# Kernel tuning notes

Measured on AMD Instinct MI355X. Metric: run time of the kernel, lower is better.

Reference implementation:

```python
import jax, jax.numpy as jnp
import numpy as np

B, L, D = 2, 2048, 1024
H, G = 16, 2            # num_heads, num_kv_groups
HPG = H // G            # heads per kv group = 8
DQK, DV = 128, 128      # qk_head_dim, v_head_dim (head_dim=64, ratios=2.0)


def setup_inputs() -> dict:
    key = jax.random.key(0)
    ks = jax.random.split(key, 12)

    def xavier(k, shape, scale=1.0):
        fan_in, fan_out = shape[0], shape[1]
        lim = np.sqrt(6.0 / (fan_in + fan_out))
        return jax.random.uniform(k, shape, jnp.float32, -lim, lim) * scale

    return {
        "in_q": jax.random.normal(ks[0], (B, L, D), jnp.float32),
        "in_k": jax.random.normal(ks[1], (B, L, D), jnp.float32),
        "in_v": jax.random.normal(ks[2], (B, L, D), jnp.float32),
        # weights stored as [in, out] (transpose of torch Linear); qk_init_scale=0.5
        "Wq": xavier(ks[3], (D, H * DQK), 0.5),
        "bq": jnp.zeros((H * DQK,), jnp.float32),
        "Wk": xavier(ks[4], (D, G * DQK), 0.5),
        "bk": jnp.zeros((G * DQK,), jnp.float32),
        "Wv": xavier(ks[5], (D, G * DV)),
        "bv": jnp.zeros((G * DV,), jnp.float32),
        "Wo": xavier(ks[6], (H * DV, D)),
        "bo": jnp.zeros((D,), jnp.float32),
        "q_extra_scale": jnp.ones((1,), jnp.float32),
    }


def reference(in_q, in_k, in_v, Wq, bq, Wk, bk, Wv, bv, Wo, bo, q_extra_scale):
    # fused projections
    q = (in_q @ Wq + bq) * q_extra_scale              # [B,L,H*DQK]
    k = in_k @ Wk + bk                                 # [B,L,G*DQK]
    v = in_v @ Wv + bv                                 # [B,L,G*DV]

    # reshape: keep GQA group structure instead of materializing repeat_interleave
    q = q.reshape(B, L, G, HPG, DQK)                   # heads grouped: head h = g*HPG + m
    k = k.reshape(B, L, G, DQK)
    v = v.reshape(B, L, G, DV)

    scale = 1.0 / np.sqrt(DQK)
    # scores: [B,G,HPG,L_q,L_kv]
    scores = jnp.einsum("bsgmd,btgd->bgmst", q, k) * scale
    causal = jnp.tril(jnp.ones((L, L), bool))          # is_causal=True
    scores = jnp.where(causal, scores, jnp.finfo(scores.dtype).min)
    attn = jax.nn.softmax(scores, axis=-1)
    ctx = jnp.einsum("bgmst,btgd->bsgmd", attn, v)     # [B,L,G,HPG,DV]
    ctx = ctx.reshape(B, L, H * DV)
    return ctx @ Wo + bo                               # [B,L,D]
```

## Files before the change

### kernel.cpp

```cpp
#include <hip/hip_runtime.h>


typedef __bf16 bf16;
typedef __bf16 bf16x8 __attribute__((ext_vector_type(8)));
typedef __bf16 bf16x4 __attribute__((ext_vector_type(4)));
typedef float f32x4 __attribute__((ext_vector_type(4)));
typedef float float4v __attribute__((ext_vector_type(4)));

#define MFMA_BF16(a, b, c) __builtin_amdgcn_mfma_f32_16x16x32_bf16((a), (b), (c), 0, 0, 0)

static constexpr int Bz = 2, Lz = 2048, Dz = 1024;
static constexpr int Hz = 16, Gz = 2;
static constexpr int DQKz = 128, DVz = 128;

__device__ __forceinline__ void async_copy16(const bf16* g, bf16* l) {
    __builtin_amdgcn_global_load_lds(
        (const __attribute__((address_space(1))) unsigned int*)g,
        (__attribute__((address_space(3))) unsigned int*)l, 16, 0, 0);
}

__global__ __launch_bounds__(256) void prep(
    const float* __restrict__ q, const float* __restrict__ k,
    const float* __restrict__ v, bf16* __restrict__ dq,
    bf16* __restrict__ dk, bf16* __restrict__ dv,
    const float* __restrict__ Wq, const float* __restrict__ Wk,
    const float* __restrict__ Wv, const float* __restrict__ Wo,
    bf16* __restrict__ WqT, bf16* __restrict__ WkT,
    bf16* __restrict__ WvT, bf16* __restrict__ WoT)
{
    int bid = blockIdx.x;
    if (bid < 6144) {
        const float* s = bid < 2048 ? q : (bid < 4096 ? k : v);
        bf16* d = bid < 2048 ? dq : (bid < 4096 ? dk : dv);
        int i = (bid & 2047) * 2048 + threadIdx.x * 8;
        float4v a = *(const float4v*)(s + i);
        float4v b = *(const float4v*)(s + i + 4);
        bf16x8 o;
        #pragma unroll
        for (int j = 0; j < 4; ++j) { o[j] = (bf16)a[j]; o[j + 4] = (bf16)b[j]; }
        *(bf16x8*)(d + i) = o;
        return;
    }
    bid -= 6144;
    const float* W; bf16* WT; int K, N;
    if (bid < 2048)      { W = Wq; WT = WqT; K = 1024; N = 2048; }
    else if (bid < 2304) { W = Wk; WT = WkT; K = 1024; N = 256;  bid -= 2048; }
    else if (bid < 2560) { W = Wv; WT = WvT; K = 1024; N = 256;  bid -= 2304; }
    else                 { W = Wo; WT = WoT; K = 2048; N = 1024; bid -= 2560; }
    int tiles_n = N >> 5;
    int n0 = (bid % tiles_n) * 32, k0 = (bid / tiles_n) * 32;

    __shared__ bf16 t[32][33];
    int tx = threadIdx.x & 31, ty = threadIdx.x >> 5;
    #pragma unroll
    for (int i = 0; i < 4; ++i)
        t[ty + i * 8][tx] = (bf16)W[(size_t)(k0 + ty + i * 8) * N + n0 + tx];
    __syncthreads();
    #pragma unroll
    for (int i = 0; i < 4; ++i)
        WT[(size_t)(n0 + ty + i * 8) * K + k0 + tx] = t[tx][ty + i * 8];
}

template <typename TC>
__device__ __forceinline__ void gemm_tile(
    const bf16* __restrict__ A, const bf16* __restrict__ BT,
    const float* __restrict__ bias, float scale, TC* __restrict__ C,
    int M, int N, int K, int m0, int n0, bool trans_out,
    bf16 (&As)[2][128 * 64], bf16 (&Bs)[2][128 * 64])
{
    const int tid  = threadIdx.x;
    const int wave = tid >> 6;
    const int lane = tid & 63;
    const int quad = lane >> 4;
    const int l16  = lane & 15;
    const int sw   = l16 & 7;
    const int wm = wave >> 2, wn = wave & 3;

    f32x4 acc[4][2] = {};

    auto stage = [&](int k0, int buf) {
        #pragma unroll
        for (int s = 0; s < 2; ++s) {
            int i = s * 512 + tid;
            int row = i >> 3, c = (i & 7) ^ (row & 7);
            async_copy16(A + (size_t)(m0 + row) * K + k0 + c * 8, &As[buf][i * 8]);
        }
        #pragma unroll
        for (int s = 0; s < 2; ++s) {
            int i = s * 512 + tid;
            int row = i >> 3, c = (i & 7) ^ (row & 7);
            async_copy16(BT + (size_t)(n0 + row) * K + k0 + c * 8, &Bs[buf][i * 8]);
        }
    };

    stage(0, 0);
    int cur = 0;
    for (int k0 = 0; k0 < K; k0 += 64) {
        __syncthreads();
        if (k0 + 64 < K) stage(k0 + 64, cur ^ 1);

        #pragma unroll
        for (int ks = 0; ks < 2; ++ks) {
            bf16x8 af[4], bfv[2];
            #pragma unroll
            for (int mt = 0; mt < 4; ++mt)
                af[mt] = *(const bf16x8*)(&As[cur][((wm * 64 + mt * 16 + l16) * 8
                                                    + ((ks * 4 + quad) ^ sw)) * 8]);
            #pragma unroll
            for (int nt = 0; nt < 2; ++nt)
                bfv[nt] = *(const bf16x8*)(&Bs[cur][((wn * 32 + nt * 16 + l16) * 8
                                                     + ((ks * 4 + quad) ^ sw)) * 8]);
            #pragma unroll
            for (int mt = 0; mt < 4; ++mt)
                #pragma unroll
                for (int nt = 0; nt < 2; ++nt)
                    acc[mt][nt] = MFMA_BF16(af[mt], bfv[nt], acc[mt][nt]);
        }
        cur ^= 1;
    }

    #pragma unroll
    for (int nt = 0; nt < 2; ++nt) {
        int col = n0 + wn * 32 + nt * 16 + l16;
        float bv = bias[col];
        #pragma unroll
        for (int mt = 0; mt < 4; ++mt) {
            int row = m0 + wm * 64 + mt * 16 + quad * 4;
            if (trans_out) {
                struct V4 { TC v[4]; } o;
                #pragma unroll
                for (int r = 0; r < 4; ++r)
                    o.v[r] = (TC)((acc[mt][nt][r] + bv) * scale);
                *(V4*)(&C[(size_t)col * M + row]) = o;
            } else {
                #pragma unroll
                for (int r = 0; r < 4; ++r)
                    C[(size_t)(row + r) * N + col] =
                        (TC)((acc[mt][nt][r] + bv) * scale);
            }
        }
    }
}

__global__ __launch_bounds__(512, 4) void proj_qkv(
    const bf16* __restrict__ aq, const bf16* __restrict__ ak,
    const bf16* __restrict__ av, const bf16* __restrict__ WqT,
    const bf16* __restrict__ WkT, const bf16* __restrict__ WvT,
    const float* __restrict__ bq, const float* __restrict__ bk,
    const float* __restrict__ bv, const float* __restrict__ qsc,
    bf16* __restrict__ Qw, bf16* __restrict__ Kw, bf16* __restrict__ VwT)
{
    __shared__ bf16 As[2][128 * 64];
    __shared__ bf16 Bs[2][128 * 64];
    int bid = blockIdx.x;
    if (bid < 512) {
        float scale = qsc[0] * 0.08838834764831845f * 1.4426950408889634f;
        gemm_tile<bf16>(aq, WqT, bq, scale, Qw, 4096, 2048, 1024,
                        (bid >> 4) * 128, (bid & 15) * 128, false, As, Bs);
    } else if (bid < 576) {
        int b2 = bid - 512;
        gemm_tile<bf16>(ak, WkT, bk, 1.0f, Kw, 4096, 256, 1024,
                        (b2 >> 1) * 128, (b2 & 1) * 128, false, As, Bs);
    } else {
        int b2 = bid - 576;
        gemm_tile<bf16>(av, WvT, bv, 1.0f, VwT, 4096, 256, 1024,
                        (b2 >> 1) * 128, (b2 & 1) * 128, true, As, Bs);
    }
}

__global__ __launch_bounds__(512, 4) void proj_o(
    const bf16* __restrict__ Cw, const bf16* __restrict__ WoT,
    const float* __restrict__ bo, float* __restrict__ out)
{
    __shared__ bf16 As[2][128 * 64];
    __shared__ bf16 Bs[2][128 * 64];
    gemm_tile<float>(Cw, WoT, bo, 1.0f, out, 4096, 1024, 2048,
                     (blockIdx.x >> 3) * 128, (blockIdx.x & 7) * 128,
                     false, As, Bs);
}

__global__ __launch_bounds__(256, 2) void attn_fused(
    const bf16* __restrict__ Q,
    const bf16* __restrict__ Kp,
    const bf16* __restrict__ VT,
    bf16* __restrict__ ctx)
{
    __shared__ bf16 Kb[2][64 * 128];
    __shared__ bf16 Vb[2][128 * 64];
    __shared__ bf16 Ps[4][16 * 72];

    const int tid  = threadIdx.x;
    const int wave = tid >> 6;
    const int lane = tid & 63;
    const int quad = lane >> 4;
    const int l16  = lane & 15;
    const int sw   = l16 & 7;

    const int h = blockIdx.y;
    const int b = blockIdx.z;
    const int g = h >> 3;

    const bf16* kgbase = Kp + (size_t)(b * Lz) * (Gz * DQKz) + g * DQKz;
    const bf16* vgbase = VT + (size_t)(g * DVz) * (Bz * Lz) + b * Lz;

    auto stage = [&](int kt, int buf) {
        const bf16* kb = kgbase + (size_t)(kt * 64) * (Gz * DQKz);
        #pragma unroll
        for (int s = 0; s < 4; ++s) {
            int i = s * 256 + tid;
            int key = i >> 4, c = (i & 15) ^ (key & 7);
            async_copy16(kb + (size_t)key * (Gz * DQKz) + c * 8, &Kb[buf][i * 8]);
        }
        const bf16* vb = vgbase + kt * 64;
        #pragma unroll
        for (int s = 0; s < 4; ++s) {
            int i = s * 256 + tid;
            int dv = i >> 3, c = (i & 7) ^ (dv & 7);
            async_copy16(vb + (size_t)dv * (Bz * Lz) + c * 8, &Vb[buf][i * 8]);
        }
    };

    for (int pass = 0; pass < 2; ++pass) {
        const int qt  = pass == 0 ? (31 - blockIdx.x) : blockIdx.x;
        const int q0  = qt * 64;
        const int nkt = qt + 1;
        const int qrow = q0 + wave * 16 + l16;

        bf16x8 qf[4];
        {
            const bf16* qbase = Q + (size_t)(b * Lz + qrow) * (Hz * DQKz) + h * DQKz;
            #pragma unroll
            for (int ks = 0; ks < 4; ++ks)
                qf[ks] = *(const bf16x8*)(qbase + ks * 32 + quad * 8);
        }

        f32x4 oacc[8] = {};
        float lsum = 0.0f;

        if (pass) __syncthreads();
        stage(0, 0);
        int cur = 0;

        bf16* ps = Ps[wave];

        for (int kt = 0; kt < nkt; ++kt) {
            __syncthreads();
            if (kt + 1 < nkt) stage(kt + 1, cur ^ 1);

            const bf16* kcur = Kb[cur];
            const bf16* vcur = Vb[cur];

            f32x4 sacc[4] = {};
            #pragma unroll
            for (int nf = 0; nf < 4; ++nf) {
                #pragma unroll
                for (int ks = 0; ks < 4; ++ks) {
                    bf16x8 kf = *(const bf16x8*)(&kcur[((nf * 16 + l16) * 16
                                                        + ((ks * 4 + quad) ^ sw)) * 8]);
                    sacc[nf] = MFMA_BF16(kf, qf[ks], sacc[nf]);
                }
            }

            float pv[4][4];
            if (kt == nkt - 1) {
                const int kv0 = kt * 64;
                #pragma unroll
                for (int nf = 0; nf < 4; ++nf) {
                    int keyb = kv0 + nf * 16 + quad * 4;
                    #pragma unroll
                    for (int r = 0; r < 4; ++r)
                        pv[nf][r] = (keyb + r > qrow) ? 0.0f
                                                      : exp2f(sacc[nf][r] - 8.0f);
                }
            } else {
                #pragma unroll
                for (int nf = 0; nf < 4; ++nf)
                    #pragma unroll
                    for (int r = 0; r < 4; ++r)
                        pv[nf][r] = exp2f(sacc[nf][r] - 8.0f);
            }

            #pragma unroll
            for (int nf = 0; nf < 4; ++nf)
                lsum += (pv[nf][0] + pv[nf][1]) + (pv[nf][2] + pv[nf][3]);

            #pragma unroll
            for (int nf = 0; nf < 4; ++nf) {
                bf16x4 pk;
                #pragma unroll
                for (int r = 0; r < 4; ++r) pk[r] = (bf16)pv[nf][r];
                *(bf16x4*)(&ps[l16 * 72 + nf * 16 + quad * 4]) = pk;
            }

            #pragma unroll
            for (int ks2 = 0; ks2 < 2; ++ks2) {
                bf16x8 pf = *(const bf16x8*)(&ps[l16 * 72 + ks2 * 32 + quad * 8]);
                #pragma unroll
                for (int nf2 = 0; nf2 < 8; ++nf2) {
                    bf16x8 vf = *(const bf16x8*)(&vcur[((nf2 * 16 + l16) * 8
                                                        + ((ks2 * 4 + quad) ^ sw)) * 8]);
                    oacc[nf2] = MFMA_BF16(vf, pf, oacc[nf2]);
                }
            }
            cur ^= 1;
        }

        lsum += __shfl_xor(lsum, 16);
        lsum += __shfl_xor(lsum, 32);
        const float inv = 1.0f / lsum;

        bf16* cbase = ctx + (size_t)(b * Lz + qrow) * (Hz * DVz) + h * DVz;
        #pragma unroll
        for (int nf2 = 0; nf2 < 8; ++nf2) {
            bf16x4 o4;
            #pragma unroll
            for (int r = 0; r < 4; ++r) o4[r] = (bf16)(oacc[nf2][r] * inv);
            *(bf16x4*)(&cbase[nf2 * 16 + quad * 4]) = o4;
        }
    }
}

extern "C" void kernel_launch(void* const* d_in, const int* in_sizes, int n_in,
                              void* d_out, int out_size, void* d_ws, size_t ws_size,
                              hipStream_t stream)
{
    (void)in_sizes; (void)n_in; (void)out_size; (void)ws_size;

    const float* in_q = (const float*)d_in[0];
    const float* in_k = (const float*)d_in[1];
    const float* in_v = (const float*)d_in[2];
    const float* Wq   = (const float*)d_in[3];
    const float* bq   = (const float*)d_in[4];
    const float* Wk   = (const float*)d_in[5];
    const float* bk   = (const float*)d_in[6];
    const float* Wv   = (const float*)d_in[7];
    const float* bv   = (const float*)d_in[8];
    const float* Wo   = (const float*)d_in[9];
    const float* bo   = (const float*)d_in[10];
    const float* qsc  = (const float*)d_in[11];
    float* out = (float*)d_out;

    const int M = Bz * Lz;
    const int NQ = Hz * DQKz;
    const int NKV = Gz * DQKz;

    bf16* aq  = (bf16*)d_ws;
    bf16* WqT = aq  + (size_t)M * Dz;
    bf16* WkT = WqT + (size_t)NQ * Dz;
    bf16* WvT = WkT + (size_t)NKV * Dz;
    bf16* WoT = WvT + (size_t)NKV * Dz;
    bf16* Qw  = WoT + (size_t)Dz * NQ;
    bf16* Kw  = Qw  + (size_t)M * NQ;
    bf16* VwT = Kw  + (size_t)M * NKV;
    bf16* Cw  = VwT + (size_t)NKV * M;
    bf16* ak  = Cw;
    bf16* av  = Cw + (size_t)M * Dz;

    prep<<<dim3(10752), dim3(256), 0, stream>>>(
        in_q, in_k, in_v, aq, ak, av, Wq, Wk, Wv, Wo, WqT, WkT, WvT, WoT);

    proj_qkv<<<dim3(640), dim3(512), 0, stream>>>(
        aq, ak, av, WqT, WkT, WvT, bq, bk, bv, qsc, Qw, Kw, VwT);

    attn_fused<<<dim3(Lz / 128, Hz, Bz), dim3(256), 0, stream>>>(Qw, Kw, VwT, Cw);

    proj_o<<<dim3(256), dim3(512), 0, stream>>>(Cw, WoT, bo, out);
}
```

Baseline: 256.4 us.

## Share K/V tiles across four heads per attention block, add XCD-aware GEMM tile mapping

The attention kernel now runs 512 threads per block. Each block covers four heads of one KV group over 32 query rows, so every K/V tile staged into LDS is reused by four heads instead of one. This cuts global and LDS staging traffic per head. The P scratch buffer switches from padding to an XOR swizzle to avoid bank conflicts, and the Q and O projection GEMMs remap block IDs so neighbouring M tiles land on the same XCD for L2 reuse. In exchange, the tighter launch bounds (512,4) could force register spills, and the grid has fewer, larger blocks.

```diff
diff --git a/kernel.cpp b/kernel.cpp
--- a/kernel.cpp
+++ b/kernel.cpp
@@ -154,9 +154,12 @@
     __shared__ bf16 Bs[2][128 * 64];
     int bid = blockIdx.x;
     if (bid < 512) {
+        int xcd = bid & 7, rest = bid >> 3;
+        int n = rest & 15, mg = rest >> 4;
+        int m = mg * 8 + xcd;
         float scale = qsc[0] * 0.08838834764831845f * 1.4426950408889634f;
         gemm_tile<bf16>(aq, WqT, bq, scale, Qw, 4096, 2048, 1024,
-                        (bid >> 4) * 128, (bid & 15) * 128, false, As, Bs);
+                        m * 128, n * 128, false, As, Bs);
     } else if (bid < 576) {
         int b2 = bid - 512;
         gemm_tile<bf16>(ak, WkT, bk, 1.0f, Kw, 4096, 256, 1024,
@@ -174,12 +177,14 @@
 {
     __shared__ bf16 As[2][128 * 64];
     __shared__ bf16 Bs[2][128 * 64];
+    int xcd = blockIdx.x & 7, rest = blockIdx.x >> 3;
+    int n = rest & 7, mg = rest >> 3;
+    int m = mg * 8 + xcd;
     gemm_tile<float>(Cw, WoT, bo, 1.0f, out, 4096, 1024, 2048,
-                     (blockIdx.x >> 3) * 128, (blockIdx.x & 7) * 128,
-                     false, As, Bs);
-}
-
-__global__ __launch_bounds__(256, 2) void attn_fused(
+                     m * 128, n * 128, false, As, Bs);
+}
+
+__global__ __launch_bounds__(512, 4) void attn_fused(
     const bf16* __restrict__ Q,
     const bf16* __restrict__ Kp,
     const bf16* __restrict__ VT,
@@ -187,7 +192,7 @@
 {
     __shared__ bf16 Kb[2][64 * 128];
     __shared__ bf16 Vb[2][128 * 64];
-    __shared__ bf16 Ps[4][16 * 72];
+    __shared__ bf16 Ps[8][16 * 64];
 
     const int tid  = threadIdx.x;
     const int wave = tid >> 6;
@@ -196,9 +201,11 @@
     const int l16  = lane & 15;
     const int sw   = l16 & 7;
 
-    const int h = blockIdx.y;
-    const int b = blockIdx.z;
-    const int g = h >> 3;
+    const int gph = blockIdx.y;
+    const int g   = gph >> 1;
+    const int h   = g * 8 + (gph & 1) * 4 + (wave >> 1);
+    const int b   = blockIdx.z;
+    const int wrow = wave & 1;
 
     const bf16* kgbase = Kp + (size_t)(b * Lz) * (Gz * DQKz) + g * DQKz;
     const bf16* vgbase = VT + (size_t)(g * DVz) * (Bz * Lz) + b * Lz;
@@ -206,25 +213,27 @@
     auto stage = [&](int kt, int buf) {
         const bf16* kb = kgbase + (size_t)(kt * 64) * (Gz * DQKz);
         #pragma unroll
-        for (int s = 0; s < 4; ++s) {
-            int i = s * 256 + tid;
+        for (int s = 0; s < 2; ++s) {
+            int i = s * 512 + tid;
             int key = i >> 4, c = (i & 15) ^ (key & 7);
             async_copy16(kb + (size_t)key * (Gz * DQKz) + c * 8, &Kb[buf][i * 8]);
         }
         const bf16* vb = vgbase + kt * 64;
         #pragma unroll
-        for (int s = 0; s < 4; ++s) {
-            int i = s * 256 + tid;
+        for (int s = 0; s < 2; ++s) {
+            int i = s * 512 + tid;
             int dv = i >> 3, c = (i & 7) ^ (dv & 7);
             async_copy16(vb + (size_t)dv * (Bz * Lz) + c * 8, &Vb[buf][i * 8]);
         }
     };
 
+    bf16* ps = Ps[wave];
+
     for (int pass = 0; pass < 2; ++pass) {
-        const int qt  = pass == 0 ? (31 - blockIdx.x) : blockIdx.x;
-        const int q0  = qt * 64;
-        const int nkt = qt + 1;
-        const int qrow = q0 + wave * 16 + l16;
+        const int qt  = pass == 0 ? (63 - blockIdx.x) : blockIdx.x;
+        const int q0  = qt * 32;
+        const int nkt = (qt >> 1) + 1;
+        const int qrow = q0 + wrow * 16 + l16;
 
         bf16x8 qf[4];
         {
@@ -240,8 +249,6 @@
         if (pass) __syncthreads();
         stage(0, 0);
         int cur = 0;
-
-        bf16* ps = Ps[wave];
 
         for (int kt = 0; kt < nkt; ++kt) {
             __syncthreads();
@@ -289,12 +296,14 @@
                 bf16x4 pk;
                 #pragma unroll
                 for (int r = 0; r < 4; ++r) pk[r] = (bf16)pv[nf][r];
-                *(bf16x4*)(&ps[l16 * 72 + nf * 16 + quad * 4]) = pk;
+                int c16 = nf * 2 + (quad >> 1);
+                *(bf16x4*)(&ps[l16 * 64 + ((c16 ^ sw) << 3) + ((quad & 1) << 2)]) = pk;
             }
 
             #pragma unroll
             for (int ks2 = 0; ks2 < 2; ++ks2) {
-                bf16x8 pf = *(const bf16x8*)(&ps[l16 * 72 + ks2 * 32 + quad * 8]);
+                bf16x8 pf = *(const bf16x8*)(&ps[l16 * 64
+                                                 + (((ks2 * 4 + quad) ^ sw) << 3)]);
                 #pragma unroll
                 for (int nf2 = 0; nf2 < 8; ++nf2) {
                     bf16x8 vf = *(const bf16x8*)(&vcur[((nf2 * 16 + l16) * 8
@@ -341,18 +350,16 @@
     float* out = (float*)d_out;
 
     const int M = Bz * Lz;
-    const int NQ = Hz * DQKz;
-    const int NKV = Gz * DQKz;
 
     bf16* aq  = (bf16*)d_ws;
     bf16* WqT = aq  + (size_t)M * Dz;
-    bf16* WkT = WqT + (size_t)NQ * Dz;
-    bf16* WvT = WkT + (size_t)NKV * Dz;
-    bf16* WoT = WvT + (size_t)NKV * Dz;
-    bf16* Qw  = WoT + (size_t)Dz * NQ;
-    bf16* Kw  = Qw  + (size_t)M * NQ;
-    bf16* VwT = Kw  + (size_t)M * NKV;
-    bf16* Cw  = VwT + (size_t)NKV * M;
+    bf16* WkT = WqT + (size_t)2048 * 1024;
+    bf16* WvT = WkT + (size_t)256 * 1024;
+    bf16* WoT = WvT + (size_t)256 * 1024;
+    bf16* Qw  = WoT + (size_t)1024 * 2048;
+    bf16* Kw  = Qw  + (size_t)M * 2048;
+    bf16* VwT = Kw  + (size_t)M * 256;
+    bf16* Cw  = VwT + (size_t)256 * M;
     bf16* ak  = Cw;
     bf16* av  = Cw + (size_t)M * Dz;
 
@@ -362,7 +369,7 @@
     proj_qkv<<<dim3(640), dim3(512), 0, stream>>>(
         aq, ak, av, WqT, WkT, WvT, bq, bk, bv, qsc, Qw, Kw, VwT);
 
-    attn_fused<<<dim3(Lz / 128, Hz, Bz), dim3(256), 0, stream>>>(Qw, Kw, VwT, Cw);
+    attn_fused<<<dim3(32, 4, 2), dim3(512), 0, stream>>>(Qw, Kw, VwT, Cw);
 
     proj_o<<<dim3(256), dim3(512), 0, stream>>>(Cw, WoT, bo, out);
 }
```

Measured after the change: 260.4 us. About the same (+1.5%).
